# Optimization experiments

Hardware: AMD Instinct MI355X
Metric: run time of the kernel (lower is better)

Reference implementation:

```python
import jax, jax.numpy as jnp
import numpy as np

B, L, D = 64, 196, 512      # batch, num annotation vectors, encoder_dim
A, M, N = 512, 512, 512     # attention_dim, embed_dim, decoder_dim
K, T_MAX = 10000, 32        # vocab_size, max caption length


def setup_inputs() -> dict:
    key = jax.random.key(0)
    ks = jax.random.split(key, 32)
    sc = 0.02

    def w(i, shape):
        return jax.random.normal(ks[i], shape, jnp.float32) * sc

    lens = jnp.sort(jax.random.randint(ks[2], (B,), 2, T_MAX + 1))[::-1]
    lens = lens.at[0].set(T_MAX)  # sorted descending; ensures max_decode_len = T_MAX-1

    return {
        "encoder_out": jax.random.normal(ks[0], (B, L, D), jnp.float32),
        "captions": jax.random.randint(ks[1], (B, T_MAX), 0, K),
        "caption_lengths": lens,
        # embedding (uniform(-0.1, 0.1) per _init_weights)
        "emb": jax.random.uniform(ks[3], (K, M), jnp.float32, -0.1, 0.1),
        # attention MLP (Show-Attend-Tell style: relu then scalar projection)
        "W_ea": w(4, (D, A)), "b_ea": jnp.zeros((A,), jnp.float32),
        "W_da": w(5, (N, A)), "b_da": jnp.zeros((A,), jnp.float32),
        "w_fa": w(6, (A,)),   "b_fa": jnp.zeros((), jnp.float32),
        # init_h / init_c
        "W_hi": w(7, (D, N)), "b_hi": jnp.zeros((N,), jnp.float32),
        "W_ci": w(8, (D, N)), "b_ci": jnp.zeros((N,), jnp.float32),
        # LSTMCell (PyTorch gate order i, f, g, o along 4N)
        "W_ih": w(9, (M + D, 4 * N)), "W_hh": w(10, (N, 4 * N)),
        "b_ih": jnp.zeros((4 * N,), jnp.float32), "b_hh": jnp.zeros((4 * N,), jnp.float32),
        # f_beta gate
        "W_fb": w(11, (N, D)), "b_fb": jnp.zeros((D,), jnp.float32),
        # deep output layers
        "W_lh": w(12, (N, M)), "b_lh": jnp.zeros((M,), jnp.float32),
        "W_lz": w(13, (D, M)), "b_lz": jnp.zeros((M,), jnp.float32),
        "W_lo": jax.random.uniform(ks[14], (M, K), jnp.float32, -0.1, 0.1),
        "b_lo": jnp.zeros((K,), jnp.float32),
    }


def reference(encoder_out, captions, caption_lengths, emb,
              W_ea, b_ea, W_da, b_da, w_fa, b_fa,
              W_hi, b_hi, W_ci, b_ci,
              W_ih, W_hh, b_ih, b_hh,
              W_fb, b_fb, W_lh, b_lh, W_lz, b_lz, W_lo, b_lo):
    # dropout is evaluated in eval mode (identity)
    T = captions.shape[1] - 1                 # max_decode_len (lengths sorted desc, max = T_MAX)
    dec_len = caption_lengths - 1             # (B,)

    mean_ann = encoder_out.mean(axis=1)       # (B, D)
    h0 = jnp.tanh(mean_ann @ W_hi + b_hi)
    c0 = jnp.tanh(mean_ann @ W_ci + b_ci)

    embs = emb[captions]                      # (B, T_MAX, M)
    emb_seq = jnp.swapaxes(embs[:, :T], 0, 1) # (T, B, M)
    att1 = encoder_out @ W_ea + b_ea          # (B, L, A) precomputed once

    def step(carry, xs):
        h, c = carry
        t, emb_t = xs
        # soft attention
        att2 = h @ W_da + b_da                              # (B, A)
        e = jax.nn.relu(att1 + att2[:, None, :]) @ w_fa + b_fa  # (B, L)
        alpha = jax.nn.softmax(e, axis=-1)
        z = jnp.einsum('bl,bld->bd', alpha, encoder_out)    # (B, D)
        beta = jax.nn.sigmoid(h @ W_fb + b_fb)
        z = beta * z
        # LSTM cell
        x = jnp.concatenate([emb_t, z], axis=1)             # (B, M+D)
        gates = x @ W_ih + h @ W_hh + b_ih + b_hh
        i, f, g, o = jnp.split(gates, 4, axis=1)
        c_new = jax.nn.sigmoid(f) * c + jax.nn.sigmoid(i) * jnp.tanh(g)
        h_new = jax.nn.sigmoid(o) * jnp.tanh(c_new)
        # deep output
        logits = (emb_t + h_new @ W_lh + b_lh + z @ W_lz + b_lz) @ W_lo + b_lo
        # ragged mask: only sequences with dec_len > t are active (emulates h[:batch_size_t])
        m = t < dec_len                                     # (B,)
        mf = m[:, None].astype(h.dtype)
        h = jnp.where(m[:, None], h_new, h)
        c = jnp.where(m[:, None], c_new, c)
        return (h, c), (logits * mf, alpha * mf)

    _, (preds, alphas) = jax.lax.scan(step, (h0, c0), (jnp.arange(T), emb_seq))
    predictions = jnp.swapaxes(preds, 0, 1)   # (B, T, K)
    alphas_out = jnp.swapaxes(alphas, 0, 1)   # (B, T, L)
    return predictions, alphas_out
```

## Files before the change

kernel.cpp:

```cpp
#include <hip/hip_runtime.h>
#include <hip/hip_bf16.h>

typedef short short8 __attribute__((ext_vector_type(8)));
typedef float floatx4 __attribute__((ext_vector_type(4)));

#define B_ 64
#define L_ 196
#define T_ 31
#define PRED_ 19840000ULL

__device__ __forceinline__ float bf2f(unsigned short u){
  union { unsigned int i; float f; } v; v.i = ((unsigned int)u)<<16; return v.f;
}
__device__ __forceinline__ float sigm(float x){ return 1.0f/(1.0f+__expf(-x)); }

__global__ __launch_bounds__(256) void k_cast(const float* __restrict__ src,
                                              __hip_bfloat16* __restrict__ dst, int n4){
  int i = blockIdx.x*256 + threadIdx.x;
  if (i < n4){
    const float4 v = *(const float4*)(src + (size_t)i*4);
    size_t o = (size_t)i*4;
    dst[o+0] = __float2bfloat16(v.x);
    dst[o+1] = __float2bfloat16(v.y);
    dst[o+2] = __float2bfloat16(v.z);
    dst[o+3] = __float2bfloat16(v.w);
  }
}

__global__ __launch_bounds__(1024) void k_trans_f32(const float* __restrict__ src,
    float* __restrict__ dst, int Kin, int Nin, int S){
  __shared__ float tile[32][33];
  int n0 = blockIdx.x*32, k0 = blockIdx.y*32;
  int x = threadIdx.x & 31, y = threadIdx.x >> 5;
  int k = k0 + y, nn = n0 + x;
  tile[y][x] = (k < Kin && nn < Nin) ? src[(size_t)k*Nin + nn] : 0.0f;
  __syncthreads();
  int n2 = n0 + y, k2 = k0 + x;
  if (n2 < Nin && k2 < Kin) dst[(size_t)n2*S + k2] = tile[x][y];
}

__global__ __launch_bounds__(1024) void k_trans_bf16(const float* __restrict__ src,
    __hip_bfloat16* __restrict__ dst, int Kin, int Nin, int S, int Rtot){
  __shared__ float tile[32][33];
  int n0 = blockIdx.x*32, k0 = blockIdx.y*32;
  int x = threadIdx.x & 31, y = threadIdx.x >> 5;
  int k = k0 + y, nn = n0 + x;
  tile[y][x] = (k < Kin && nn < Nin) ? src[(size_t)k*Nin + nn] : 0.0f;
  __syncthreads();
  int n2 = n0 + y, k2 = k0 + x;
  if (n2 < Rtot && k2 < Kin) dst[(size_t)n2*S + k2] = __float2bfloat16(tile[x][y]);
}

__global__ __launch_bounds__(512) void k_emb(const int* __restrict__ captions,
    const float* __restrict__ emb, float* __restrict__ ET, __hip_bfloat16* __restrict__ Erow){
  int tb = blockIdx.x; int t = tb >> 6; int b = tb & 63; int m = threadIdx.x;
  int cap = captions[b*32 + t];
  float v = emb[(size_t)cap*512 + m];
  ET[((size_t)t*512 + m)*64 + b] = v;
  Erow[((size_t)(t*64 + b))*512 + m] = __float2bfloat16(v);
}

__global__ __launch_bounds__(512) void k_init(const float* __restrict__ enc,
    const float* __restrict__ Whi, const float* __restrict__ bhi,
    const float* __restrict__ Wci, const float* __restrict__ bci,
    float* __restrict__ hT, float* __restrict__ cT){
  int b = blockIdx.x; int d = threadIdx.x;
  __shared__ float ms[512];
  const float* eb = enc + (size_t)b*L_*512;
  float s = 0.f;
  for (int l = 0; l < L_; l++) s += eb[(size_t)l*512 + d];
  ms[d] = s * (1.0f/196.0f);
  __syncthreads();
  float a1 = bhi[d], a2 = bci[d];
  #pragma unroll 4
  for (int k = 0; k < 512; k++){
    float mv = ms[k];
    a1 += mv * Whi[(size_t)k*512 + d];
    a2 += mv * Wci[(size_t)k*512 + d];
  }
  hT[d*64 + b] = tanhf(a1);
  cT[d*64 + b] = tanhf(a2);
}

__global__ __launch_bounds__(256) void k_phase1(const float* __restrict__ hT,
    const float* __restrict__ W1T, const float* __restrict__ b_da,
    const float* __restrict__ b_fb, float* __restrict__ ph1T){
  int lane = threadIdx.x & 63;
  int gw = (blockIdx.x << 2) + (threadIdx.x >> 6);
  gw = __builtin_amdgcn_readfirstlane(gw);
  const float* __restrict__ wp0 = W1T + (size_t)(gw*4+0)*512;
  const float* __restrict__ wp1 = W1T + (size_t)(gw*4+1)*512;
  const float* __restrict__ wp2 = W1T + (size_t)(gw*4+2)*512;
  const float* __restrict__ wp3 = W1T + (size_t)(gw*4+3)*512;
  float a0=0.f, a1=0.f, a2=0.f, a3=0.f;
  #pragma unroll 8
  for (int k = 0; k < 512; k++){
    float h = hT[k*64 + lane];
    a0 += h * wp0[k]; a1 += h * wp1[k]; a2 += h * wp2[k]; a3 += h * wp3[k];
  }
  float acc[4] = {a0, a1, a2, a3};
  #pragma unroll
  for (int c = 0; c < 4; c++){
    int n = gw*4 + c;
    float bias = (n < 512) ? b_da[n] : ((n < 1024) ? b_fb[n-512] : 0.f);
    ph1T[(size_t)n*64 + lane] = acc[c] + bias;
  }
}

__global__ __launch_bounds__(256) void k_attn(const float* __restrict__ enc,
    const __hip_bfloat16* __restrict__ att1, const float* __restrict__ ph1T,
    const float* __restrict__ wfa, const int* __restrict__ caplen, int t,
    float* __restrict__ zT, __hip_bfloat16* __restrict__ HZ, float* __restrict__ outAlpha){
  int b = blockIdx.x;
  int tid = threadIdx.x; int lane = tid & 63; int w = tid >> 6;
  __shared__ float es[196];
  __shared__ float MS[2];
  float a2r[8], wfr[8];
  #pragma unroll
  for (int u = 0; u < 8; u++){
    int a = lane*8 + u;
    a2r[u] = ph1T[(size_t)a*64 + b];
    wfr[u] = wfa[a];
  }
  const unsigned short* at1 = (const unsigned short*)att1 + (size_t)b*L_*512;
  for (int l = w; l < L_; l += 4){
    short8 s = *(const short8*)(at1 + (size_t)l*512 + lane*8);
    float e = 0.f;
    #pragma unroll
    for (int u = 0; u < 8; u++){
      float v = bf2f((unsigned short)s[u]) + a2r[u];
      v = fmaxf(v, 0.f);
      e += v * wfr[u];
    }
    #pragma unroll
    for (int off = 32; off; off >>= 1) e += __shfl_xor(e, off, 64);
    if (lane == 0) es[l] = e;
  }
  __syncthreads();
  if (w == 0){
    float v0 = es[lane], v1 = es[lane+64], v2 = es[lane+128];
    float v3 = (lane < 4) ? es[lane+192] : -1e30f;
    float m = fmaxf(fmaxf(v0, v1), fmaxf(v2, v3));
    #pragma unroll
    for (int off = 32; off; off >>= 1) m = fmaxf(m, __shfl_xor(m, off, 64));
    float sm = __expf(v0-m) + __expf(v1-m) + __expf(v2-m) + ((lane < 4) ? __expf(v3-m) : 0.f);
    #pragma unroll
    for (int off = 32; off; off >>= 1) sm += __shfl_xor(sm, off, 64);
    if (lane == 0){ MS[0] = m; MS[1] = sm; }
  }
  __syncthreads();
  float mx = MS[0]; float inv = 1.0f / MS[1];
  int dl = caplen[b] - 1;
  float maskf = (t < dl) ? 1.f : 0.f;
  float* oa = outAlpha + ((size_t)b*T_ + t)*L_;
  for (int l = tid; l < L_; l += 256){
    float al = __expf(es[l] - mx) * inv;
    es[l] = al;
    oa[l] = al * maskf;
  }
  __syncthreads();
  int d0 = tid, d1 = tid + 256;
  const float* eb = enc + (size_t)b*L_*512;
  float z0 = 0.f, z1 = 0.f;
  #pragma unroll 2
  for (int l = 0; l < L_; l++){
    float al = es[l];
    z0 += al * eb[(size_t)l*512 + d0];
    z1 += al * eb[(size_t)l*512 + d1];
  }
  float bp0 = ph1T[(size_t)(512+d0)*64 + b];
  float bp1 = ph1T[(size_t)(512+d1)*64 + b];
  z0 *= sigm(bp0);
  z1 *= sigm(bp1);
  zT[d0*64 + b] = z0;
  zT[d1*64 + b] = z1;
  __hip_bfloat16* hz = HZ + ((size_t)(t*64 + b))*1024 + 512;
  hz[d0] = __float2bfloat16(z0);
  hz[d1] = __float2bfloat16(z1);
}

__global__ __launch_bounds__(256) void k_gates(const float* __restrict__ ET,
    const float* __restrict__ zT, const float* __restrict__ WihT,
    const float* __restrict__ ph1T, const float* __restrict__ b_ih,
    const float* __restrict__ b_hh, const int* __restrict__ caplen, int t,
    float* __restrict__ hT, float* __restrict__ cT, __hip_bfloat16* __restrict__ HZ){
  int tid = threadIdx.x; int lane = tid & 63; int w = tid >> 6;
  int n = blockIdx.x*2 + (w >> 1);
  n = __builtin_amdgcn_readfirstlane(n);
  int kh = w & 1;
  const float* __restrict__ x0 = (kh == 0) ? (ET + (size_t)t*512*64) : zT;
  const float* __restrict__ wq0 = WihT + ((size_t)(0*512 + n))*1024 + kh*512;
  const float* __restrict__ wq1 = WihT + ((size_t)(1*512 + n))*1024 + kh*512;
  const float* __restrict__ wq2 = WihT + ((size_t)(2*512 + n))*1024 + kh*512;
  const float* __restrict__ wq3 = WihT + ((size_t)(3*512 + n))*1024 + kh*512;
  float g0=0.f, g1=0.f, g2=0.f, g3=0.f;
  #pragma unroll 8
  for (int k = 0; k < 512; k++){
    float x = x0[k*64 + lane];
    g0 += x * wq0[k]; g1 += x * wq1[k]; g2 += x * wq2[k]; g3 += x * wq3[k];
  }
  __shared__ float gs[4][4][64];
  gs[w][0][lane] = g0; gs[w][1][lane] = g1; gs[w][2][lane] = g2; gs[w][3][lane] = g3;
  __syncthreads();
  if (kh == 0){
    int wo = w + 1;
    float gi = g0 + gs[wo][0][lane] + ph1T[(size_t)(1024 + 0*512 + n)*64 + lane] + b_ih[0*512+n] + b_hh[0*512+n];
    float gf = g1 + gs[wo][1][lane] + ph1T[(size_t)(1024 + 1*512 + n)*64 + lane] + b_ih[1*512+n] + b_hh[1*512+n];
    float gg = g2 + gs[wo][2][lane] + ph1T[(size_t)(1024 + 2*512 + n)*64 + lane] + b_ih[2*512+n] + b_hh[2*512+n];
    float go = g3 + gs[wo][3][lane] + ph1T[(size_t)(1024 + 3*512 + n)*64 + lane] + b_ih[3*512+n] + b_hh[3*512+n];
    float i_ = sigm(gi), f_ = sigm(gf), c_in = tanhf(gg), o_ = sigm(go);
    float c_old = cT[n*64 + lane];
    float c_new = f_ * c_old + i_ * c_in;
    float h_new = o_ * tanhf(c_new);
    float h_old = hT[n*64 + lane];
    int dl = caplen[lane] - 1;
    bool m = (t < dl);
    hT[n*64 + lane] = m ? h_new : h_old;
    cT[n*64 + lane] = m ? c_new : c_old;
    HZ[((size_t)(t*64 + lane))*1024 + n] = __float2bfloat16(h_new);
  }
}

__global__ __launch_bounds__(256) void k_gemm(const __hip_bfloat16* __restrict__ Abf,
    const __hip_bfloat16* __restrict__ Bt, int K, int mode, int Nreal,
    const float* __restrict__ bias1, const float* __restrict__ bias2,
    const __hip_bfloat16* __restrict__ Erow, const int* __restrict__ caplen,
    __hip_bfloat16* __restrict__ outB, float* __restrict__ outF){
  int lane = threadIdx.x & 63; int wv = threadIdx.x >> 6;
  int wr = wv >> 1, wc = wv & 1;
  int r0 = blockIdx.y*64 + wr*32;
  int c0 = blockIdx.x*64 + wc*32;
  int l15 = lane & 15, lg = lane >> 4;
  const short* Ap = (const short*)Abf;
  const short* Bp = (const short*)Bt;
  floatx4 acc00 = {0,0,0,0}, acc01 = {0,0,0,0}, acc10 = {0,0,0,0}, acc11 = {0,0,0,0};
  size_t ar0 = (size_t)(r0 + l15)*K + lg*8;
  size_t ar1 = ar0 + (size_t)16*K;
  size_t br0 = (size_t)(c0 + l15)*K + lg*8;
  size_t br1 = br0 + (size_t)16*K;
  #pragma unroll 4
  for (int k0 = 0; k0 < K; k0 += 32){
    short8 av0 = *(const short8*)(Ap + ar0 + k0);
    short8 av1 = *(const short8*)(Ap + ar1 + k0);
    short8 bv0 = *(const short8*)(Bp + br0 + k0);
    short8 bv1 = *(const short8*)(Bp + br1 + k0);
    acc00 = __builtin_amdgcn_mfma_f32_16x16x32_bf16(av0, bv0, acc00, 0, 0, 0);
    acc01 = __builtin_amdgcn_mfma_f32_16x16x32_bf16(av0, bv1, acc01, 0, 0, 0);
    acc10 = __builtin_amdgcn_mfma_f32_16x16x32_bf16(av1, bv0, acc10, 0, 0, 0);
    acc11 = __builtin_amdgcn_mfma_f32_16x16x32_bf16(av1, bv1, acc11, 0, 0, 0);
  }
  floatx4 accs[2][2] = {{acc00, acc01}, {acc10, acc11}};
  #pragma unroll
  for (int i = 0; i < 2; i++){
    #pragma unroll
    for (int j = 0; j < 2; j++){
      #pragma unroll
      for (int v = 0; v < 4; v++){
        int r = r0 + 16*i + lg*4 + v;
        int c = c0 + 16*j + l15;
        float val = accs[i][j][v];
        if (mode == 0){
          outB[(size_t)r*512 + c] = __float2bfloat16(val + bias1[c]);
        } else if (mode == 1){
          float e = bf2f(((const unsigned short*)Erow)[(size_t)r*512 + c]);
          outB[(size_t)r*512 + c] = __float2bfloat16(val + bias1[c] + bias2[c] + e);
        } else {
          if (c < Nreal){
            int t = r >> 6, b = r & 63;
            float mf = (t < caplen[b] - 1) ? 1.f : 0.f;
            outF[((size_t)b*T_ + t)*10000 + c] = (val + bias1[c]) * mf;
          }
        }
      }
    }
  }
}

extern "C" void kernel_launch(void* const* d_in, const int* in_sizes, int n_in,
                              void* d_out, int out_size, void* d_ws, size_t ws_size,
                              hipStream_t stream){
  (void)in_sizes; (void)n_in; (void)out_size; (void)ws_size;
  const float* enc   = (const float*)d_in[0];
  const int* captions = (const int*)d_in[1];
  const int* caplen  = (const int*)d_in[2];
  const float* emb   = (const float*)d_in[3];
  const float* W_ea  = (const float*)d_in[4];  const float* b_ea = (const float*)d_in[5];
  const float* W_da  = (const float*)d_in[6];  const float* b_da = (const float*)d_in[7];
  const float* w_fa  = (const float*)d_in[8];
  const float* W_hi  = (const float*)d_in[10]; const float* b_hi = (const float*)d_in[11];
  const float* W_ci  = (const float*)d_in[12]; const float* b_ci = (const float*)d_in[13];
  const float* W_ih  = (const float*)d_in[14]; const float* W_hh = (const float*)d_in[15];
  const float* b_ih  = (const float*)d_in[16]; const float* b_hh = (const float*)d_in[17];
  const float* W_fb  = (const float*)d_in[18]; const float* b_fb = (const float*)d_in[19];
  const float* W_lh  = (const float*)d_in[20]; const float* b_lh = (const float*)d_in[21];
  const float* W_lz  = (const float*)d_in[22]; const float* b_lz = (const float*)d_in[23];
  const float* W_lo  = (const float*)d_in[24]; const float* b_lo = (const float*)d_in[25];
  float* out = (float*)d_out;

  char* p = (char*)d_ws;
  auto alloc = [&](size_t bytes){ char* r = p; p += bytes; return r; };
  __hip_bfloat16* enc_bf  = (__hip_bfloat16*)alloc(12845056);
  __hip_bfloat16* att1_bf = (__hip_bfloat16*)alloc(12845056);
  __hip_bfloat16* WeaT    = (__hip_bfloat16*)alloc(524288);
  float*          W1T     = (float*)alloc(6291456);
  float*          WihT    = (float*)alloc(8388608);
  __hip_bfloat16* W2T     = (__hip_bfloat16*)alloc(1048576);
  __hip_bfloat16* WloT    = (__hip_bfloat16*)alloc(10289152);
  float*          ET      = (float*)alloc(4063232);
  __hip_bfloat16* Erow    = (__hip_bfloat16*)alloc(2031616);
  __hip_bfloat16* HZ      = (__hip_bfloat16*)alloc(4063232);
  __hip_bfloat16* Ubf     = (__hip_bfloat16*)alloc(2031616);
  float*          hT      = (float*)alloc(131072);
  float*          cT      = (float*)alloc(131072);
  float*          zT      = (float*)alloc(131072);
  float*          ph1T    = (float*)alloc(786432);

  k_cast<<<dim3(6272), dim3(256), 0, stream>>>(enc, enc_bf, 1605632);
  k_trans_f32<<<dim3(16, 16), dim3(1024), 0, stream>>>(W_da, W1T,             512, 512,  512);
  k_trans_f32<<<dim3(16, 16), dim3(1024), 0, stream>>>(W_fb, W1T + 512*512,   512, 512,  512);
  k_trans_f32<<<dim3(64, 16), dim3(1024), 0, stream>>>(W_hh, W1T + 1024*512,  512, 2048, 512);
  k_trans_f32<<<dim3(64, 32), dim3(1024), 0, stream>>>(W_ih, WihT,           1024, 2048, 1024);
  k_trans_bf16<<<dim3(16, 16), dim3(1024), 0, stream>>>(W_ea, WeaT,       512, 512,   512,  512);
  k_trans_bf16<<<dim3(16, 16), dim3(1024), 0, stream>>>(W_lh, W2T,        512, 512,   1024, 512);
  k_trans_bf16<<<dim3(16, 16), dim3(1024), 0, stream>>>(W_lz, W2T + 512,  512, 512,   1024, 512);
  k_trans_bf16<<<dim3(314, 16), dim3(1024), 0, stream>>>(W_lo, WloT,      512, 10000, 512,  10048);
  k_emb<<<dim3(1984), dim3(512), 0, stream>>>(captions, emb, ET, Erow);
  k_init<<<dim3(64), dim3(512), 0, stream>>>(enc, W_hi, b_hi, W_ci, b_ci, hT, cT);

  k_gemm<<<dim3(8, 196), dim3(256), 0, stream>>>(enc_bf, WeaT, 512, 0, 512,
      b_ea, nullptr, nullptr, nullptr, att1_bf, nullptr);

  for (int t = 0; t < T_; t++){
    k_phase1<<<dim3(192), dim3(256), 0, stream>>>(hT, W1T, b_da, b_fb, ph1T);
    k_attn<<<dim3(64), dim3(256), 0, stream>>>(enc, att1_bf, ph1T, w_fa, caplen, t,
        zT, HZ, out + PRED_);
    k_gates<<<dim3(256), dim3(256), 0, stream>>>(ET, zT, WihT, ph1T, b_ih, b_hh,
        caplen, t, hT, cT, HZ);
  }

  k_gemm<<<dim3(8, 31), dim3(256), 0, stream>>>(HZ, W2T, 1024, 1, 512,
      b_lh, b_lz, Erow, nullptr, Ubf, nullptr);
  k_gemm<<<dim3(157, 31), dim3(256), 0, stream>>>(Ubf, WloT, 512, 2, 10000,
      b_lo, nullptr, nullptr, caplen, nullptr, out);
}
```

Baseline: 3.704 ms.

## Fuse recurrent decode loop into one persistent cooperative kernel with grid syncs

Replaces the per-timestep launches of phase1, attention and gates with a single cooperative kernel of 256 blocks. Each block keeps its slice of the W_da/W_fb/W_hh/W_ih rows resident in shared memory as fp32 and exchanges h and z as packed bf16 through global memory, with grid.sync between stages. The embedding half of the input-to-hidden projection is precomputed for all timesteps by a batched GEMM. Attention is split across four blocks per batch row using partial softmax that is merged afterwards, and att1 is stored transposed. Weights and the recurrent state exchanges now use bf16, which reduces precision, and the kernel relies on all 256 blocks being co-resident.

```diff
diff --git a/kernel.cpp b/kernel.cpp
--- a/kernel.cpp
+++ b/kernel.cpp
@@ -1,5 +1,8 @@
 #include <hip/hip_runtime.h>
 #include <hip/hip_bf16.h>
+#include <hip/hip_cooperative_groups.h>
+
+namespace cg = cooperative_groups;
 
 typedef short short8 __attribute__((ext_vector_type(8)));
 typedef float floatx4 __attribute__((ext_vector_type(4)));
@@ -11,6 +14,17 @@
 
 __device__ __forceinline__ float bf2f(unsigned short u){
   union { unsigned int i; float f; } v; v.i = ((unsigned int)u)<<16; return v.f;
+}
+__device__ __forceinline__ float lo16(unsigned int u){
+  union { unsigned int i; float f; } v; v.i = u << 16; return v.f;
+}
+__device__ __forceinline__ float hi16(unsigned int u){
+  union { unsigned int i; float f; } v; v.i = u & 0xffff0000u; return v.f;
+}
+__device__ __forceinline__ unsigned int pk2(float a, float b){
+  union { __hip_bfloat16 h; unsigned short u; } x, y;
+  x.h = __float2bfloat16(a); y.h = __float2bfloat16(b);
+  return (unsigned int)x.u | ((unsigned int)y.u << 16);
 }
 __device__ __forceinline__ float sigm(float x){ return 1.0f/(1.0f+__expf(-x)); }
 
@@ -27,18 +41,6 @@
   }
 }
 
-__global__ __launch_bounds__(1024) void k_trans_f32(const float* __restrict__ src,
-    float* __restrict__ dst, int Kin, int Nin, int S){
-  __shared__ float tile[32][33];
-  int n0 = blockIdx.x*32, k0 = blockIdx.y*32;
-  int x = threadIdx.x & 31, y = threadIdx.x >> 5;
-  int k = k0 + y, nn = n0 + x;
-  tile[y][x] = (k < Kin && nn < Nin) ? src[(size_t)k*Nin + nn] : 0.0f;
-  __syncthreads();
-  int n2 = n0 + y, k2 = k0 + x;
-  if (n2 < Nin && k2 < Kin) dst[(size_t)n2*S + k2] = tile[x][y];
-}
-
 __global__ __launch_bounds__(1024) void k_trans_bf16(const float* __restrict__ src,
     __hip_bfloat16* __restrict__ dst, int Kin, int Nin, int S, int Rtot){
   __shared__ float tile[32][33];
@@ -52,20 +54,19 @@
 }
 
 __global__ __launch_bounds__(512) void k_emb(const int* __restrict__ captions,
-    const float* __restrict__ emb, float* __restrict__ ET, __hip_bfloat16* __restrict__ Erow){
+    const float* __restrict__ emb, __hip_bfloat16* __restrict__ Erow){
   int tb = blockIdx.x; int t = tb >> 6; int b = tb & 63; int m = threadIdx.x;
   int cap = captions[b*32 + t];
-  float v = emb[(size_t)cap*512 + m];
-  ET[((size_t)t*512 + m)*64 + b] = v;
-  Erow[((size_t)(t*64 + b))*512 + m] = __float2bfloat16(v);
+  Erow[((size_t)(t*64 + b))*512 + m] = __float2bfloat16(emb[(size_t)cap*512 + m]);
 }
 
 __global__ __launch_bounds__(512) void k_init(const float* __restrict__ enc,
     const float* __restrict__ Whi, const float* __restrict__ bhi,
     const float* __restrict__ Wci, const float* __restrict__ bci,
-    float* __restrict__ hT, float* __restrict__ cT){
+    float* __restrict__ hT, float* __restrict__ cT, unsigned int* __restrict__ hP){
   int b = blockIdx.x; int d = threadIdx.x;
   __shared__ float ms[512];
+  __shared__ float hs[512];
   const float* eb = enc + (size_t)b*L_*512;
   float s = 0.f;
   for (int l = 0; l < L_; l++) s += eb[(size_t)l*512 + d];
@@ -78,147 +79,12 @@
     a1 += mv * Whi[(size_t)k*512 + d];
     a2 += mv * Wci[(size_t)k*512 + d];
   }
-  hT[d*64 + b] = tanhf(a1);
+  float h = tanhf(a1);
+  hT[d*64 + b] = h;
   cT[d*64 + b] = tanhf(a2);
-}
-
-__global__ __launch_bounds__(256) void k_phase1(const float* __restrict__ hT,
-    const float* __restrict__ W1T, const float* __restrict__ b_da,
-    const float* __restrict__ b_fb, float* __restrict__ ph1T){
-  int lane = threadIdx.x & 63;
-  int gw = (blockIdx.x << 2) + (threadIdx.x >> 6);
-  gw = __builtin_amdgcn_readfirstlane(gw);
-  const float* __restrict__ wp0 = W1T + (size_t)(gw*4+0)*512;
-  const float* __restrict__ wp1 = W1T + (size_t)(gw*4+1)*512;
-  const float* __restrict__ wp2 = W1T + (size_t)(gw*4+2)*512;
-  const float* __restrict__ wp3 = W1T + (size_t)(gw*4+3)*512;
-  float a0=0.f, a1=0.f, a2=0.f, a3=0.f;
-  #pragma unroll 8
-  for (int k = 0; k < 512; k++){
-    float h = hT[k*64 + lane];
-    a0 += h * wp0[k]; a1 += h * wp1[k]; a2 += h * wp2[k]; a3 += h * wp3[k];
-  }
-  float acc[4] = {a0, a1, a2, a3};
-  #pragma unroll
-  for (int c = 0; c < 4; c++){
-    int n = gw*4 + c;
-    float bias = (n < 512) ? b_da[n] : ((n < 1024) ? b_fb[n-512] : 0.f);
-    ph1T[(size_t)n*64 + lane] = acc[c] + bias;
-  }
-}
-
-__global__ __launch_bounds__(256) void k_attn(const float* __restrict__ enc,
-    const __hip_bfloat16* __restrict__ att1, const float* __restrict__ ph1T,
-    const float* __restrict__ wfa, const int* __restrict__ caplen, int t,
-    float* __restrict__ zT, __hip_bfloat16* __restrict__ HZ, float* __restrict__ outAlpha){
-  int b = blockIdx.x;
-  int tid = threadIdx.x; int lane = tid & 63; int w = tid >> 6;
-  __shared__ float es[196];
-  __shared__ float MS[2];
-  float a2r[8], wfr[8];
-  #pragma unroll
-  for (int u = 0; u < 8; u++){
-    int a = lane*8 + u;
-    a2r[u] = ph1T[(size_t)a*64 + b];
-    wfr[u] = wfa[a];
-  }
-  const unsigned short* at1 = (const unsigned short*)att1 + (size_t)b*L_*512;
-  for (int l = w; l < L_; l += 4){
-    short8 s = *(const short8*)(at1 + (size_t)l*512 + lane*8);
-    float e = 0.f;
-    #pragma unroll
-    for (int u = 0; u < 8; u++){
-      float v = bf2f((unsigned short)s[u]) + a2r[u];
-      v = fmaxf(v, 0.f);
-      e += v * wfr[u];
-    }
-    #pragma unroll
-    for (int off = 32; off; off >>= 1) e += __shfl_xor(e, off, 64);
-    if (lane == 0) es[l] = e;
-  }
+  hs[d] = h;
   __syncthreads();
-  if (w == 0){
-    float v0 = es[lane], v1 = es[lane+64], v2 = es[lane+128];
-    float v3 = (lane < 4) ? es[lane+192] : -1e30f;
-    float m = fmaxf(fmaxf(v0, v1), fmaxf(v2, v3));
-    #pragma unroll
-    for (int off = 32; off; off >>= 1) m = fmaxf(m, __shfl_xor(m, off, 64));
-    float sm = __expf(v0-m) + __expf(v1-m) + __expf(v2-m) + ((lane < 4) ? __expf(v3-m) : 0.f);
-    #pragma unroll
-    for (int off = 32; off; off >>= 1) sm += __shfl_xor(sm, off, 64);
-    if (lane == 0){ MS[0] = m; MS[1] = sm; }
-  }
-  __syncthreads();
-  float mx = MS[0]; float inv = 1.0f / MS[1];
-  int dl = caplen[b] - 1;
-  float maskf = (t < dl) ? 1.f : 0.f;
-  float* oa = outAlpha + ((size_t)b*T_ + t)*L_;
-  for (int l = tid; l < L_; l += 256){
-    float al = __expf(es[l] - mx) * inv;
-    es[l] = al;
-    oa[l] = al * maskf;
-  }
-  __syncthreads();
-  int d0 = tid, d1 = tid + 256;
-  const float* eb = enc + (size_t)b*L_*512;
-  float z0 = 0.f, z1 = 0.f;
-  #pragma unroll 2
-  for (int l = 0; l < L_; l++){
-    float al = es[l];
-    z0 += al * eb[(size_t)l*512 + d0];
-    z1 += al * eb[(size_t)l*512 + d1];
-  }
-  float bp0 = ph1T[(size_t)(512+d0)*64 + b];
-  float bp1 = ph1T[(size_t)(512+d1)*64 + b];
-  z0 *= sigm(bp0);
-  z1 *= sigm(bp1);
-  zT[d0*64 + b] = z0;
-  zT[d1*64 + b] = z1;
-  __hip_bfloat16* hz = HZ + ((size_t)(t*64 + b))*1024 + 512;
-  hz[d0] = __float2bfloat16(z0);
-  hz[d1] = __float2bfloat16(z1);
-}
-
-__global__ __launch_bounds__(256) void k_gates(const float* __restrict__ ET,
-    const float* __restrict__ zT, const float* __restrict__ WihT,
-    const float* __restrict__ ph1T, const float* __restrict__ b_ih,
-    const float* __restrict__ b_hh, const int* __restrict__ caplen, int t,
-    float* __restrict__ hT, float* __restrict__ cT, __hip_bfloat16* __restrict__ HZ){
-  int tid = threadIdx.x; int lane = tid & 63; int w = tid >> 6;
-  int n = blockIdx.x*2 + (w >> 1);
-  n = __builtin_amdgcn_readfirstlane(n);
-  int kh = w & 1;
-  const float* __restrict__ x0 = (kh == 0) ? (ET + (size_t)t*512*64) : zT;
-  const float* __restrict__ wq0 = WihT + ((size_t)(0*512 + n))*1024 + kh*512;
-  const float* __restrict__ wq1 = WihT + ((size_t)(1*512 + n))*1024 + kh*512;
-  const float* __restrict__ wq2 = WihT + ((size_t)(2*512 + n))*1024 + kh*512;
-  const float* __restrict__ wq3 = WihT + ((size_t)(3*512 + n))*1024 + kh*512;
-  float g0=0.f, g1=0.f, g2=0.f, g3=0.f;
-  #pragma unroll 8
-  for (int k = 0; k < 512; k++){
-    float x = x0[k*64 + lane];
-    g0 += x * wq0[k]; g1 += x * wq1[k]; g2 += x * wq2[k]; g3 += x * wq3[k];
-  }
-  __shared__ float gs[4][4][64];
-  gs[w][0][lane] = g0; gs[w][1][lane] = g1; gs[w][2][lane] = g2; gs[w][3][lane] = g3;
-  __syncthreads();
-  if (kh == 0){
-    int wo = w + 1;
-    float gi = g0 + gs[wo][0][lane] + ph1T[(size_t)(1024 + 0*512 + n)*64 + lane] + b_ih[0*512+n] + b_hh[0*512+n];
-    float gf = g1 + gs[wo][1][lane] + ph1T[(size_t)(1024 + 1*512 + n)*64 + lane] + b_ih[1*512+n] + b_hh[1*512+n];
-    float gg = g2 + gs[wo][2][lane] + ph1T[(size_t)(1024 + 2*512 + n)*64 + lane] + b_ih[2*512+n] + b_hh[2*512+n];
-    float go = g3 + gs[wo][3][lane] + ph1T[(size_t)(1024 + 3*512 + n)*64 + lane] + b_ih[3*512+n] + b_hh[3*512+n];
-    float i_ = sigm(gi), f_ = sigm(gf), c_in = tanhf(gg), o_ = sigm(go);
-    float c_old = cT[n*64 + lane];
-    float c_new = f_ * c_old + i_ * c_in;
-    float h_new = o_ * tanhf(c_new);
-    float h_old = hT[n*64 + lane];
-    int dl = caplen[lane] - 1;
-    bool m = (t < dl);
-    hT[n*64 + lane] = m ? h_new : h_old;
-    cT[n*64 + lane] = m ? c_new : c_old;
-    HZ[((size_t)(t*64 + lane))*1024 + n] = __float2bfloat16(h_new);
-  }
+  if (d < 256) hP[d*64 + b] = pk2(hs[2*d], hs[2*d+1]);
 }
 
 __global__ __launch_bounds__(256) void k_gemm(const __hip_bfloat16* __restrict__ Abf,
@@ -260,19 +126,224 @@
         int c = c0 + 16*j + l15;
         float val = accs[i][j][v];
         if (mode == 0){
-          outB[(size_t)r*512 + c] = __float2bfloat16(val + bias1[c]);
+          unsigned int bq = ((unsigned int)r * 21400u) >> 22;
+          int l = r - (int)bq*196;
+          outB[((size_t)bq*512 + c)*196 + l] = __float2bfloat16(val + bias1[c]);
         } else if (mode == 1){
           float e = bf2f(((const unsigned short*)Erow)[(size_t)r*512 + c]);
           outB[(size_t)r*512 + c] = __float2bfloat16(val + bias1[c] + bias2[c] + e);
-        } else {
+        } else if (mode == 2){
           if (c < Nreal){
             int t = r >> 6, b = r & 63;
             float mf = (t < caplen[b] - 1) ? 1.f : 0.f;
             outF[((size_t)b*T_ + t)*10000 + c] = (val + bias1[c]) * mf;
           }
+        } else {
+          outB[((size_t)(r >> 6)*2048 + c)*64 + (r & 63)] = __float2bfloat16(val);
         }
       }
     }
+  }
+}
+
+__global__ __launch_bounds__(256, 1) void k_loop(
+    const __hip_bfloat16* __restrict__ W1Tbf,
+    const __hip_bfloat16* __restrict__ WihzT,
+    const __hip_bfloat16* __restrict__ preIH,
+    const __hip_bfloat16* __restrict__ att1T,
+    const __hip_bfloat16* __restrict__ enc_bf,
+    const float* __restrict__ wfa,
+    const float* __restrict__ b_da, const float* __restrict__ b_fb,
+    const float* __restrict__ b_ih, const float* __restrict__ b_hh,
+    const float* __restrict__ hT0, const float* __restrict__ cT0,
+    unsigned int* __restrict__ hP,
+    unsigned int* __restrict__ zP,
+    float* __restrict__ att2g,
+    float* __restrict__ betag,
+    float* __restrict__ zpart,
+    float* __restrict__ msq,
+    __hip_bfloat16* __restrict__ HZ,
+    const int* __restrict__ caplen,
+    float* __restrict__ outAlpha)
+{
+  cg::grid_group grid = cg::this_grid();
+  int tid = threadIdx.x, lane = tid & 63, w = tid >> 6;
+  int blk = blockIdx.x;
+  int n0 = blk*2;
+  int ab_base = blk*4;
+  int ab_row = ab_base + w;
+  int bb = blk >> 2, qq = blk & 3;
+
+  __shared__ float wAB[4][512];
+  __shared__ float wHH[8][512];
+  __shared__ float wZ[8][512];
+  __shared__ float wfa_l[512];
+  __shared__ float att2c[512];
+  __shared__ float eacc[4][64];
+  __shared__ float p_l[64];
+  __shared__ float glds[4][2][64];
+  __shared__ float hst[2][64], cst[2][64];
+  __shared__ float bsum[4][2];
+
+  const short* w1s = (const short*)W1Tbf;
+  const short* wzs = (const short*)WihzT;
+  for (int i = tid; i < 2048; i += 256)
+    ((float*)wAB)[i] = bf2f((unsigned short)w1s[(size_t)ab_base*512 + i]);
+  for (int i = tid; i < 4096; i += 256){
+    int g = i >> 10, j = (i >> 9) & 1, k = i & 511;
+    ((float*)wHH)[i] = bf2f((unsigned short)w1s[(size_t)(1024 + g*512 + n0 + j)*512 + k]);
+    ((float*)wZ)[i]  = bf2f((unsigned short)wzs[(size_t)(g*512 + n0 + j)*512 + k]);
+  }
+  for (int i = tid; i < 512; i += 256) wfa_l[i] = wfa[i];
+  if (tid < 128){ int j = tid >> 6;
+    hst[j][lane] = hT0[(n0+j)*64 + lane];
+    cst[j][lane] = cT0[(n0+j)*64 + lane];
+  }
+  if (tid < 8){ int g = tid >> 1, j = tid & 1;
+    bsum[g][j] = b_ih[g*512 + n0 + j] + b_hh[g*512 + n0 + j];
+  }
+  int dl  = caplen[lane] - 1;
+  int dlb = caplen[bb] - 1;
+  float biasAB = (ab_row < 512) ? b_da[ab_row] : b_fb[ab_row - 512];
+  __syncthreads();
+
+  float whh0 = 0.f, whh1 = 0.f;
+
+  for (int t = 0; t < T_; t++){
+    {
+      const float4* wa4 = (const float4*)&wAB[w][0];
+      const float4* w04 = (const float4*)&wHH[w*2+0][0];
+      const float4* w14 = (const float4*)&wHH[w*2+1][0];
+      float ab = 0.f, ga = 0.f, gb = 0.f;
+      #pragma unroll 4
+      for (int k4 = 0; k4 < 128; k4++){
+        float4 a  = wa4[k4];
+        float4 c0 = w04[k4];
+        float4 c1 = w14[k4];
+        unsigned int u0 = hP[(k4*2+0)*64 + lane];
+        unsigned int u1 = hP[(k4*2+1)*64 + lane];
+        float h0 = lo16(u0), h1 = hi16(u0), h2 = lo16(u1), h3 = hi16(u1);
+        ab += h0*a.x  + h1*a.y  + h2*a.z  + h3*a.w;
+        ga += h0*c0.x + h1*c0.y + h2*c0.z + h3*c0.w;
+        gb += h0*c1.x + h1*c1.y + h2*c1.z + h3*c1.w;
+      }
+      if (ab_row < 512) att2g[ab_row*64 + lane] = ab + biasAB;
+      else              betag[(ab_row-512)*64 + lane] = ab + biasAB;
+      whh0 = ga; whh1 = gb;
+    }
+    grid.sync();
+
+    for (int i = tid; i < 512; i += 256) att2c[i] = att2g[i*64 + bb];
+    __syncthreads();
+    {
+      float e = 0.f;
+      if (lane < 49){
+        const short* arow = (const short*)att1T + ((size_t)bb*512 + w*128)*196 + qq*49 + lane;
+        #pragma unroll 4
+        for (int a = 0; a < 128; a++){
+          float v = bf2f((unsigned short)arow[(size_t)a*196]) + att2c[w*128 + a];
+          v = fmaxf(v, 0.f);
+          e += v * wfa_l[w*128 + a];
+        }
+      }
+      eacc[w][lane] = e;
+    }
+    __syncthreads();
+    if (w == 0){
+      float ee = eacc[0][lane] + eacc[1][lane] + eacc[2][lane] + eacc[3][lane];
+      float m = (lane < 49) ? ee : -3e38f;
+      #pragma unroll
+      for (int off = 32; off; off >>= 1) m = fmaxf(m, __shfl_xor(m, off, 64));
+      float pe = (lane < 49) ? __expf(ee - m) : 0.f;
+      float s = pe;
+      #pragma unroll
+      for (int off = 32; off; off >>= 1) s += __shfl_xor(s, off, 64);
+      p_l[lane] = pe;
+      if (lane == 0){ msq[(bb*4+qq)*2+0] = m; msq[(bb*4+qq)*2+1] = s; }
+    }
+    __syncthreads();
+    {
+      float z0 = 0.f, z1 = 0.f;
+      const short* ebase = (const short*)enc_bf + ((size_t)bb*196 + qq*49)*512;
+      #pragma unroll 2
+      for (int l = 0; l < 49; l++){
+        float pl = p_l[l];
+        z0 += pl * bf2f((unsigned short)ebase[(size_t)l*512 + tid]);
+        z1 += pl * bf2f((unsigned short)ebase[(size_t)l*512 + tid + 256]);
+      }
+      zpart[(size_t)(bb*4+qq)*512 + tid]       = z0;
+      zpart[(size_t)(bb*4+qq)*512 + tid + 256] = z1;
+    }
+    grid.sync();
+
+    {
+      float m0 = msq[(bb*4+0)*2], s0 = msq[(bb*4+0)*2+1];
+      float m1 = msq[(bb*4+1)*2], s1 = msq[(bb*4+1)*2+1];
+      float m2 = msq[(bb*4+2)*2], s2 = msq[(bb*4+2)*2+1];
+      float m3 = msq[(bb*4+3)*2], s3 = msq[(bb*4+3)*2+1];
+      float M = fmaxf(fmaxf(m0,m1), fmaxf(m2,m3));
+      float c0 = __expf(m0-M), c1 = __expf(m1-M), c2 = __expf(m2-M), c3 = __expf(m3-M);
+      float inv = 1.f / (s0*c0 + s1*c1 + s2*c2 + s3*c3);
+      float mf = (t < dlb) ? 1.f : 0.f;
+      if (tid < 49){
+        float cq = (qq==0) ? c0 : (qq==1) ? c1 : (qq==2) ? c2 : c3;
+        outAlpha[((size_t)bb*T_ + t)*196 + qq*49 + tid] = p_l[tid] * cq * inv * mf;
+      }
+      if (tid < 64){
+        int d2 = qq*64 + tid;
+        int d = d2*2;
+        float za = (zpart[(size_t)(bb*4+0)*512 + d]*c0 + zpart[(size_t)(bb*4+1)*512 + d]*c1
+                  + zpart[(size_t)(bb*4+2)*512 + d]*c2 + zpart[(size_t)(bb*4+3)*512 + d]*c3) * inv;
+        float zb = (zpart[(size_t)(bb*4+0)*512 + d+1]*c0 + zpart[(size_t)(bb*4+1)*512 + d+1]*c1
+                  + zpart[(size_t)(bb*4+2)*512 + d+1]*c2 + zpart[(size_t)(bb*4+3)*512 + d+1]*c3) * inv;
+        za *= sigm(betag[d*64 + bb]);
+        zb *= sigm(betag[(d+1)*64 + bb]);
+        unsigned int pk = pk2(za, zb);
+        zP[d2*64 + bb] = pk;
+        *(unsigned int*)((short*)HZ + ((size_t)(t*64+bb)*1024 + 512 + d)) = pk;
+      }
+    }
+    grid.sync();
+
+    {
+      const float4* z04 = (const float4*)&wZ[w*2+0][0];
+      const float4* z14 = (const float4*)&wZ[w*2+1][0];
+      float g0 = whh0 + bsum[w][0];
+      float g1 = whh1 + bsum[w][1];
+      #pragma unroll 4
+      for (int k4 = 0; k4 < 128; k4++){
+        float4 c0 = z04[k4];
+        float4 c1 = z14[k4];
+        unsigned int u0 = zP[(k4*2+0)*64 + lane];
+        unsigned int u1 = zP[(k4*2+1)*64 + lane];
+        float v0 = lo16(u0), v1 = hi16(u0), v2 = lo16(u1), v3 = hi16(u1);
+        g0 += v0*c0.x + v1*c0.y + v2*c0.z + v3*c0.w;
+        g1 += v0*c1.x + v1*c1.y + v2*c1.z + v3*c1.w;
+      }
+      g0 += bf2f(((const unsigned short*)preIH)[((size_t)t*2048 + w*512 + n0+0)*64 + lane]);
+      g1 += bf2f(((const unsigned short*)preIH)[((size_t)t*2048 + w*512 + n0+1)*64 + lane]);
+      glds[w][0][lane] = g0;
+      glds[w][1][lane] = g1;
+    }
+    __syncthreads();
+    if (w < 2){
+      int j = w;
+      float gi = glds[0][j][lane], gf = glds[1][j][lane];
+      float gg = glds[2][j][lane], go = glds[3][j][lane];
+      float c_old = cst[j][lane];
+      float c_new = sigm(gf)*c_old + sigm(gi)*tanhf(gg);
+      float h_new = sigm(go)*tanhf(c_new);
+      bool mm = (t < dl);
+      float hpub = mm ? h_new : hst[j][lane];
+      cst[j][lane] = mm ? c_new : c_old;
+      hst[j][lane] = hpub;
+      HZ[((size_t)(t*64+lane))*1024 + (n0+j)] = __float2bfloat16(h_new);
+    }
+    __syncthreads();
+    if (w == 0){
+      hP[blk*64 + lane] = pk2(hst[0][lane], hst[1][lane]);
+    }
+    grid.sync();
   }
 }
 
@@ -280,10 +351,10 @@
                               void* d_out, int out_size, void* d_ws, size_t ws_size,
                               hipStream_t stream){
   (void)in_sizes; (void)n_in; (void)out_size; (void)ws_size;
-  const float* enc   = (const float*)d_in[0];
+  const float* enc    = (const float*)d_in[0];
   const int* captions = (const int*)d_in[1];
-  const int* caplen  = (const int*)d_in[2];
-  const float* emb   = (const float*)d_in[3];
+  const int* caplen   = (const int*)d_in[2];
+  const float* emb    = (const float*)d_in[3];
   const float* W_ea  = (const float*)d_in[4];  const float* b_ea = (const float*)d_in[5];
   const float* W_da  = (const float*)d_in[6];  const float* b_da = (const float*)d_in[7];
   const float* w_fa  = (const float*)d_in[8];
@@ -298,44 +369,57 @@
   float* out = (float*)d_out;
 
   char* p = (char*)d_ws;
-  auto alloc = [&](size_t bytes){ char* r = p; p += bytes; return r; };
-  __hip_bfloat16* enc_bf  = (__hip_bfloat16*)alloc(12845056);
-  __hip_bfloat16* att1_bf = (__hip_bfloat16*)alloc(12845056);
-  __hip_bfloat16* WeaT    = (__hip_bfloat16*)alloc(524288);
-  float*          W1T     = (float*)alloc(6291456);
-  float*          WihT    = (float*)alloc(8388608);
-  __hip_bfloat16* W2T     = (__hip_bfloat16*)alloc(1048576);
-  __hip_bfloat16* WloT    = (__hip_bfloat16*)alloc(10289152);
-  float*          ET      = (float*)alloc(4063232);
-  __hip_bfloat16* Erow    = (__hip_bfloat16*)alloc(2031616);
-  __hip_bfloat16* HZ      = (__hip_bfloat16*)alloc(4063232);
-  __hip_bfloat16* Ubf     = (__hip_bfloat16*)alloc(2031616);
-  float*          hT      = (float*)alloc(131072);
-  float*          cT      = (float*)alloc(131072);
-  float*          zT      = (float*)alloc(131072);
-  float*          ph1T    = (float*)alloc(786432);
+  auto alloc = [&](size_t bytes){ char* r = p; p += (bytes + 255) & ~(size_t)255; return r; };
+  __hip_bfloat16* enc_bf = (__hip_bfloat16*)alloc(12845056);
+  __hip_bfloat16* att1T  = (__hip_bfloat16*)alloc(12845056);
+  __hip_bfloat16* WeaT   = (__hip_bfloat16*)alloc(524288);
+  __hip_bfloat16* W1Tbf  = (__hip_bfloat16*)alloc(3145728);
+  __hip_bfloat16* WihzT  = (__hip_bfloat16*)alloc(2097152);
+  __hip_bfloat16* WtopT  = (__hip_bfloat16*)alloc(2097152);
+  __hip_bfloat16* W2T    = (__hip_bfloat16*)alloc(1048576);
+  __hip_bfloat16* WloT   = (__hip_bfloat16*)alloc(10289152);
+  __hip_bfloat16* Erow   = (__hip_bfloat16*)alloc(2031616);
+  __hip_bfloat16* preIH  = (__hip_bfloat16*)alloc(8126464);
+  __hip_bfloat16* HZ     = (__hip_bfloat16*)alloc(4063232);
+  __hip_bfloat16* Ubf    = (__hip_bfloat16*)alloc(2031616);
+  float*        hT0    = (float*)alloc(131072);
+  float*        cT0    = (float*)alloc(131072);
+  unsigned int* hP     = (unsigned int*)alloc(65536);
+  unsigned int* zP     = (unsigned int*)alloc(65536);
+  float*        att2g  = (float*)alloc(131072);
+  float*        betag  = (float*)alloc(131072);
+  float*        zpart  = (float*)alloc(524288);
+  float*        msq    = (float*)alloc(2048);
 
   k_cast<<<dim3(6272), dim3(256), 0, stream>>>(enc, enc_bf, 1605632);
-  k_trans_f32<<<dim3(16, 16), dim3(1024), 0, stream>>>(W_da, W1T,             512, 512,  512);
-  k_trans_f32<<<dim3(16, 16), dim3(1024), 0, stream>>>(W_fb, W1T + 512*512,   512, 512,  512);
-  k_trans_f32<<<dim3(64, 16), dim3(1024), 0, stream>>>(W_hh, W1T + 1024*512,  512, 2048, 512);
-  k_trans_f32<<<dim3(64, 32), dim3(1024), 0, stream>>>(W_ih, WihT,           1024, 2048, 1024);
-  k_trans_bf16<<<dim3(16, 16), dim3(1024), 0, stream>>>(W_ea, WeaT,       512, 512,   512,  512);
-  k_trans_bf16<<<dim3(16, 16), dim3(1024), 0, stream>>>(W_lh, W2T,        512, 512,   1024, 512);
-  k_trans_bf16<<<dim3(16, 16), dim3(1024), 0, stream>>>(W_lz, W2T + 512,  512, 512,   1024, 512);
-  k_trans_bf16<<<dim3(314, 16), dim3(1024), 0, stream>>>(W_lo, WloT,      512, 10000, 512,  10048);
-  k_emb<<<dim3(1984), dim3(512), 0, stream>>>(captions, emb, ET, Erow);
-  k_init<<<dim3(64), dim3(512), 0, stream>>>(enc, W_hi, b_hi, W_ci, b_ci, hT, cT);
+  k_trans_bf16<<<dim3(16, 16), dim3(1024), 0, stream>>>(W_ea, WeaT, 512, 512, 512, 512);
+  k_trans_bf16<<<dim3(16, 16), dim3(1024), 0, stream>>>(W_da, W1Tbf,            512, 512,  512, 512);
+  k_trans_bf16<<<dim3(16, 16), dim3(1024), 0, stream>>>(W_fb, W1Tbf + 512*512,  512, 512,  512, 512);
+  k_trans_bf16<<<dim3(64, 16), dim3(1024), 0, stream>>>(W_hh, W1Tbf + 1024*512, 512, 2048, 512, 2048);
+  k_trans_bf16<<<dim3(64, 16), dim3(1024), 0, stream>>>(W_ih, WtopT,            512, 2048, 512, 2048);
+  k_trans_bf16<<<dim3(64, 16), dim3(1024), 0, stream>>>(W_ih + 512*2048, WihzT, 512, 2048, 512, 2048);
+  k_trans_bf16<<<dim3(16, 16), dim3(1024), 0, stream>>>(W_lh, W2T,       512, 512,   1024, 512);
+  k_trans_bf16<<<dim3(16, 16), dim3(1024), 0, stream>>>(W_lz, W2T + 512, 512, 512,   1024, 512);
+  k_trans_bf16<<<dim3(314, 16), dim3(1024), 0, stream>>>(W_lo, WloT,     512, 10000, 512,  10048);
+  k_emb<<<dim3(1984), dim3(512), 0, stream>>>(captions, emb, Erow);
+  k_init<<<dim3(64), dim3(512), 0, stream>>>(enc, W_hi, b_hi, W_ci, b_ci, hT0, cT0, hP);
 
   k_gemm<<<dim3(8, 196), dim3(256), 0, stream>>>(enc_bf, WeaT, 512, 0, 512,
-      b_ea, nullptr, nullptr, nullptr, att1_bf, nullptr);
-
-  for (int t = 0; t < T_; t++){
-    k_phase1<<<dim3(192), dim3(256), 0, stream>>>(hT, W1T, b_da, b_fb, ph1T);
-    k_attn<<<dim3(64), dim3(256), 0, stream>>>(enc, att1_bf, ph1T, w_fa, caplen, t,
-        zT, HZ, out + PRED_);
-    k_gates<<<dim3(256), dim3(256), 0, stream>>>(ET, zT, WihT, ph1T, b_ih, b_hh,
-        caplen, t, hT, cT, HZ);
+      b_ea, nullptr, nullptr, nullptr, att1T, nullptr);
+  k_gemm<<<dim3(32, 31), dim3(256), 0, stream>>>(Erow, WtopT, 512, 3, 2048,
+      nullptr, nullptr, nullptr, nullptr, preIH, nullptr);
+
+  {
+    const __hip_bfloat16 *a0 = W1Tbf, *a1 = WihzT, *a2 = preIH, *a3 = att1T, *a4 = enc_bf;
+    const float *f0 = w_fa, *f1 = b_da, *f2 = b_fb, *f3 = b_ih, *f4 = b_hh, *f5 = hT0, *f6 = cT0;
+    unsigned int *u0 = hP, *u1 = zP;
+    float *g0 = att2g, *g1 = betag, *g2 = zpart, *g3 = msq;
+    __hip_bfloat16 *hz = HZ;
+    const int* cl = caplen;
+    float* oa = out + PRED_;
+    void* args[] = { &a0,&a1,&a2,&a3,&a4, &f0,&f1,&f2,&f3,&f4,&f5,&f6,
+                     &u0,&u1, &g0,&g1,&g2,&g3, &hz, &cl, &oa };
+    hipLaunchCooperativeKernel((const void*)k_loop, dim3(256), dim3(256), args, 0, stream);
   }
 
   k_gemm<<<dim3(8, 31), dim3(256), 0, stream>>>(HZ, W2T, 1024, 1, 512,
```

Result: slower. 5.728 ms (+54.6%).
